# Optimization experiments

Measured on AMD Instinct MI355X. Metric: run time of the kernel, lower is better.

Reference implementation:

```python
import jax, jax.numpy as jnp
from jax import lax
import numpy as np


def hac_round(X, W):
    """Avg-linkage HAC build+cut rounding of fractional SDP matrix X (D,D).
    Returns the 0/1 symmetric round_matrix with 1-diagonal."""
    D = X.shape[0]
    dt = X.dtype
    MAXD = jnp.max(jnp.abs(X)) * 1000.0  # _MAX_DIST sentinel
    max_sim = jnp.max(X)                 # max_similarity passed by forward()
    tril_mask = jnp.tril(jnp.ones((D, D), dtype=bool))
    # use_similarities=True branch: Y = MAXD*tril + (max_sim - X).triu(1)
    Y = jnp.where(tril_mask, MAXD, max_sim - X)
    values = jnp.min(Y, axis=1)
    indices = jnp.argmin(Y, axis=1)
    parents = jnp.arange(2 * D - 1)
    p2i = jnp.arange(2 * D - 1)   # parent_to_idx
    i2p = jnp.arange(D)           # idx_to_parent
    cs = jnp.ones(2 * D - 1, dtype=dt)
    energy = jnp.zeros(2 * D - 1, dtype=dt)
    clustering = jnp.zeros((2 * D - 1, D), dtype=dt)
    clustering = clustering.at[jnp.arange(D), jnp.arange(D)].set(jnp.arange(1, D + 1, dtype=dt))
    R = jnp.eye(D, dtype=dt)

    def body(i, st):
        Y, values, indices, parents, p2i, i2p, cs, energy, clustering, R = st
        max_node = D + i
        m1 = jnp.argmin(values)
        m2 = indices[m1]
        p1 = i2p[p2i[i2p[m1]]]
        p2 = i2p[p2i[i2p[m2]]]
        parents = parents.at[p1].set(max_node).at[p2].set(max_node)
        i2p = i2p.at[m1].set(max_node)
        p2i = p2i.at[max_node].set(m1)
        max_mask = Y == MAXD
        cs1, cs2 = cs[p1], cs[p2]
        ncs = cs1 + cs2
        cs = cs.at[max_node].set(ncs)
        # weighted average-linkage merged distances
        newv = (jnp.minimum(Y[m1, :], Y[:, m1]) * cs1 + jnp.minimum(Y[:, m2], Y[m2, :]) * cs2) / ncs
        Y = Y.at[:, m1].set(newv).at[m1, :].set(newv)
        Y = jnp.where(max_mask, MAXD, Y)
        Y = Y.at[:, m2].set(MAXD).at[m2, :].set(MAXD)
        values = values.at[m2].set(MAXD)
        vmask = values == MAXD
        values = jnp.where(vmask, MAXD, jnp.min(Y, axis=1))
        indices = jnp.argmin(Y, axis=1)
        # cut decision for the new internal node
        crow = clustering[p1] + clustering[p2]
        leaf = crow > 0                      # membership of new cluster
        lf = leaf.astype(dt)
        merge_e = lf @ (W @ lf)              # sum of W over leaf x leaf pairs
        e_sum = energy[p1] + energy[p2]
        take = merge_e >= e_sum
        energy = energy.at[max_node].set(jnp.where(take, merge_e, e_sum))
        crow = jnp.where(take & leaf, (max_node).astype(dt), crow)
        clustering = clustering.at[max_node].set(crow)
        R = jnp.where(take & (leaf[:, None] & leaf[None, :]), jnp.asarray(1.0, dt), R)
        return (Y, values, indices, parents, p2i, i2p, cs, energy, clustering, R)

    st = (Y, values, indices, parents, p2i, i2p, cs, energy, clustering, R)
    st = lax.fori_loop(0, D - 1, body, st)
    return st[-1]


def setup_inputs() -> dict:
    key = jax.random.key(0)
    k1, k2 = jax.random.split(key)
    D = 1024
    A = jax.random.uniform(k1, (D, D), dtype=jnp.float32)
    X = 0.5 * (A + A.T)                      # symmetric fractional decisions
    X = X.at[jnp.arange(D), jnp.arange(D)].set(1.0)  # 1-diagonal
    W = jnp.triu(jax.random.normal(k2, (D, D), dtype=jnp.float32), 1)  # triu(1) weights
    return {"X": X, "W": W}


def reference(X, W):
    # straight-through estimator: hard rounded solution, identity gradient w.r.t. X
    R = hac_round(X, W)
    return X + lax.stop_gradient(R - X)
```

## Files before the change

kernel.cpp:

```cpp
#include <hip/hip_runtime.h>
#include <stdint.h>

#define D 1024

typedef unsigned long long u64;
typedef unsigned int u32;

__device__ __forceinline__ u32 enc_f(float f) {
    u32 b = __float_as_uint(f);
    return (b & 0x80000000u) ? ~b : (b | 0x80000000u);
}
__device__ __forceinline__ float dec_f(u32 u) {
    u32 b = (u & 0x80000000u) ? (u ^ 0x80000000u) : ~u;
    return __uint_as_float(b);
}

__global__ void k_maxred(const float* __restrict__ X, u32* scal) {
    float mx = -INFINITY, ma = 0.f;
    int stride = gridDim.x * blockDim.x;
    for (int i = blockIdx.x * blockDim.x + threadIdx.x; i < D * D; i += stride) {
        float v = X[i];
        mx = fmaxf(mx, v);
        ma = fmaxf(ma, fabsf(v));
    }
    for (int o = 32; o; o >>= 1) {
        mx = fmaxf(mx, __shfl_xor(mx, o));
        ma = fmaxf(ma, __shfl_xor(ma, o));
    }
    if ((threadIdx.x & 63) == 0) {
        atomicMax(&scal[0], enc_f(mx));
        atomicMax(&scal[1], enc_f(ma));
    }
}

__global__ void k_init(const float* __restrict__ X, const float* __restrict__ W,
                       float* __restrict__ dist, float* __restrict__ cross,
                       const u32* __restrict__ scal) {
    int idx = blockIdx.x * blockDim.x + threadIdx.x;
    if (idx >= D * D) return;
    float max_sim = dec_f(scal[0]);
    float MAXD = __fmul_rn(dec_f(scal[1]), 1000.0f);
    int i = idx >> 10, j = idx & (D - 1);
    float x = X[idx];
    dist[idx] = (i == j) ? MAXD : __fsub_rn(max_sim, x);
    cross[idx] = (i == j) ? 0.0f : (W[idx] + W[j * D + i]);
}

__global__ void k_rowmin(const float* __restrict__ dist, float* __restrict__ values_g,
                         int* __restrict__ indices_g, const u32* __restrict__ scal) {
    int r = blockIdx.x;
    int lane = threadIdx.x;
    float MAXD = __fmul_rn(dec_f(scal[1]), 1000.0f);
    u64 best = ((u64)__float_as_uint(MAXD) << 32);
    const float* row = dist + (size_t)r * D;
    for (int j = lane; j < D; j += 64) {
        if (j > r) {
            u64 k = ((u64)__float_as_uint(row[j]) << 32) | (u32)j;
            if (k < best) best = k;
        }
    }
    for (int o = 32; o; o >>= 1) {
        u64 k2 = __shfl_xor(best, o);
        if (k2 < best) best = k2;
    }
    if (lane == 0) {
        values_g[r] = __uint_as_float((u32)(best >> 32));
        indices_g[r] = (int)(best & 0xffffffffu);
    }
}

__global__ void __launch_bounds__(1024) k_hac(
        float* __restrict__ dist, float* __restrict__ cross,
        const float* __restrict__ values_g, const int* __restrict__ indices_g,
        int* __restrict__ labels_g, const u32* __restrict__ scal) {
    __shared__ __align__(16) float values_l[D];
    __shared__ float values_stage[D];
    __shared__ int indices_l[D];
    __shared__ __align__(16) float newv_l[D];
    __shared__ float cs_l[D];
    __shared__ unsigned char dead_l[D];
    __shared__ unsigned char marked_l[D];
    __shared__ int slot_l[D];
    __shared__ int label_l[D];
    __shared__ double within_l[D];
    __shared__ double energy_l[D];
    __shared__ int rlist[2][D];
    __shared__ int nrec[2];
    __shared__ u64 s_best[2];
    __shared__ float s_cross12;
    __shared__ int s_takeP, s_m1P, s_labP;

    const int t = threadIdx.x;
    const int lane = t & 63, wid = t >> 6;
    const float MAXD = __fmul_rn(dec_f(scal[1]), 1000.0f);
    const u32 MAXDb = __float_as_uint(MAXD);

    values_l[t] = values_g[t];
    indices_l[t] = indices_g[t];
    cs_l[t] = 1.0f;
    dead_l[t] = 0;
    marked_l[t] = 0;
    slot_l[t] = t;
    label_l[t] = t;
    within_l[t] = 0.0;
    energy_l[t] = 0.0;
    if (t == 0) {
        s_takeP = 0; s_m1P = -1; s_labP = 0;
        nrec[0] = 0; nrec[1] = 0;
        s_best[0] = ~0ull; s_best[1] = ~0ull;
    }
    __syncthreads();
    {
        u64 key = ((u64)__float_as_uint(values_l[t]) << 32) | ((u32)t << 10) |
                  (u32)indices_l[t];
        for (int o = 32; o; o >>= 1) {
            u64 k2 = __shfl_xor(key, o);
            if (k2 < key) key = k2;
        }
        if (lane == 0) atomicMin(&s_best[0], key);
    }
    __syncthreads();

    for (int it = 0; it < D - 1; ++it) {
        const int cb = it & 1, pb = cb ^ 1;

        const u64 bk = s_best[cb];
        const int m1 = (int)((bk >> 10) & 1023);
        const int m2 = (int)(bk & 1023);
        const float cs1 = cs_l[m1], cs2 = cs_l[m2];
        const float ncs = __fadd_rn(cs1, cs2);
        const int pm1 = s_m1P;
        if (t == 0) s_best[pb] = ~0ull;

        if (marked_l[t]) { values_l[t] = values_stage[t]; marked_l[t] = 0; }
        if (t == m2) {
            dead_l[m2] = 1;
            values_l[m2] = MAXD;
            indices_l[m2] = 0;
        }
        const bool alive = !dead_l[t];

        float d1, d2, c1, c2;
        if (alive || t == m2) {
            d1 = dist[(size_t)m1 * D + t];
            d2 = dist[(size_t)m2 * D + t];
            c1 = cross[(size_t)m1 * D + t];
            c2 = cross[(size_t)m2 * D + t];
        }

        {
            int sl = slot_l[t];
            if (s_takeP && sl == pm1) label_l[t] = s_labP;
            if (sl == m2) slot_l[t] = m1;
        }

        float nv = MAXD, ncx = 0.0f;
        bool do_st = false;
        {
            if (t == m2) s_cross12 = c1;
            if (alive && t != m1) {
                nv = __fdiv_rn(__fadd_rn(__fmul_rn(d1, cs1), __fmul_rn(d2, cs2)), ncs);
                ncx = c1 + c2;
                dist[(size_t)m1 * D + t] = nv;
                cross[(size_t)m1 * D + t] = ncx;
                do_st = true;
            }
            newv_l[t] = nv;
        }
        {
            float v = values_l[t];
            if (t == m1) {
                values_l[t] = MAXD;
                marked_l[t] = 1;
            } else if (alive && v < MAXD) {
                int idx = indices_l[t];
                if (idx == m2) {
                    rlist[cb][atomicAdd(&nrec[cb], 1)] = t;
                    values_l[t] = MAXD;
                    marked_l[t] = 1;
                } else if (idx == m1) {
                    if (nv <= v) values_l[t] = nv;
                    else {
                        rlist[cb][atomicAdd(&nrec[cb], 1)] = t;
                        values_l[t] = MAXD;
                        marked_l[t] = 1;
                    }
                } else if (t < m1) {
                    if (nv < v) { values_l[t] = nv; indices_l[t] = m1; }
                    else if (nv == v && m1 < idx) indices_l[t] = m1;
                }
            }
        }
        __syncthreads();

        if (do_st) {
            dist[(size_t)t * D + m1] = nv;
            cross[(size_t)t * D + m1] = ncx;
        }
        if (t == m1) cs_l[m1] = ncs;
        const int n = nrec[cb];
        if (t == 0) nrec[pb] = 0;

        if (wid == 0) {
            if (lane == 0) {
                double merge_e = within_l[m1] + within_l[m2] + (double)s_cross12;
                double e_sum = energy_l[m1] + energy_l[m2];
                int take = (merge_e >= e_sum) ? 1 : 0;
                within_l[m1] = merge_e;
                energy_l[m1] = take ? merge_e : e_sum;
                s_takeP = take;
                s_m1P = m1;
                s_labP = D + it;
            }
            const float4* v4 = (const float4*)values_l;
            u64 bb = ~0ull;
#pragma unroll
            for (int c = 0; c < 4; ++c) {
                int fi = lane + 64 * c;
                float4 q = v4[fi];
                int b = fi << 2;
                u64 k;
                k = ((u64)__float_as_uint(q.x) << 32) | (u32)(b + 0); if (k < bb) bb = k;
                k = ((u64)__float_as_uint(q.y) << 32) | (u32)(b + 1); if (k < bb) bb = k;
                k = ((u64)__float_as_uint(q.z) << 32) | (u32)(b + 2); if (k < bb) bb = k;
                k = ((u64)__float_as_uint(q.w) << 32) | (u32)(b + 3); if (k < bb) bb = k;
            }
            for (int o = 32; o; o >>= 1) {
                u64 k2 = __shfl_xor(bb, o);
                if (k2 < bb) bb = k2;
            }
            if (lane == 0) {
                int r = (int)(bb & 1023);
                int idx = indices_l[r];
                atomicMin(&s_best[pb],
                          (bb & 0xffffffff00000000ull) | ((u32)r << 10) | (u32)idx);
            }
        } else if (wid == 1) {
            u64 bb = ((u64)MAXDb << 32);
            const float4* nv4 = (const float4*)newv_l;
            for (int c = lane; c < D / 4; c += 64) {
                float4 q = nv4[c];
                int j0 = c << 2;
#pragma unroll
                for (int e = 0; e < 4; ++e) {
                    int j = j0 + e;
                    float dv = (e == 0) ? q.x : (e == 1) ? q.y : (e == 2) ? q.z : q.w;
                    if (j > m1) {
                        u64 k = ((u64)__float_as_uint(dv) << 32) | (u32)j;
                        if (k < bb) bb = k;
                    }
                }
            }
            for (int o = 32; o; o >>= 1) {
                u64 k2 = __shfl_xor(bb, o);
                if (k2 < bb) bb = k2;
            }
            if (lane == 0) {
                values_stage[m1] = __uint_as_float((u32)(bb >> 32));
                indices_l[m1] = (int)(bb & 0xffffffffu);
                atomicMin(&s_best[pb],
                          (bb & 0xffffffff00000000ull) | ((u32)m1 << 10) | (bb & 1023));
            }
        } else {
            for (int q = wid - 2; q < n; q += 14) {
                const int r = rlist[cb][q];
                const float subst = newv_l[r];
                u64 bb = ((u64)MAXDb << 32);
                const float4* row4 = (const float4*)(dist + (size_t)r * D);
                for (int c = lane; c < D / 4; c += 64) {
                    float4 q4 = row4[c];
                    int j0 = c << 2;
#pragma unroll
                    for (int e = 0; e < 4; ++e) {
                        int j = j0 + e;
                        float dv = (e == 0) ? q4.x : (e == 1) ? q4.y : (e == 2) ? q4.z : q4.w;
                        if (j == m1) dv = subst;
                        if (j > r && !dead_l[j]) {
                            u64 k = ((u64)__float_as_uint(dv) << 32) | (u32)j;
                            if (k < bb) bb = k;
                        }
                    }
                }
                for (int o = 32; o; o >>= 1) {
                    u64 k2 = __shfl_xor(bb, o);
                    if (k2 < bb) bb = k2;
                }
                if (lane == 0) {
                    values_stage[r] = __uint_as_float((u32)(bb >> 32));
                    indices_l[r] = (int)(bb & 0xffffffffu);
                    atomicMin(&s_best[pb],
                              (bb & 0xffffffff00000000ull) | ((u32)r << 10) | (bb & 1023));
                }
            }
        }
        __syncthreads();
    }

    {
        int lab = label_l[t];
        if (s_takeP && slot_l[t] == s_m1P) lab = s_labP;
        labels_g[t] = lab;
    }
}

__global__ void k_out(const int* __restrict__ labels, float* __restrict__ out) {
    int idx = blockIdx.x * blockDim.x + threadIdx.x;
    if (idx >= D * D) return;
    int i = idx >> 10, j = idx & (D - 1);
    out[idx] = (i == j || labels[i] == labels[j]) ? 1.0f : 0.0f;
}

extern "C" void kernel_launch(void* const* d_in, const int* in_sizes, int n_in,
                              void* d_out, int out_size, void* d_ws, size_t ws_size,
                              hipStream_t stream) {
    const float* X = (const float*)d_in[0];
    const float* W = (const float*)d_in[1];

    char* ws = (char*)d_ws;
    const size_t MAT_BYTES = (size_t)D * D * sizeof(float);
    float* dist = (float*)ws;
    float* cross = (float*)(ws + MAT_BYTES);
    float* values_g = (float*)(ws + 2 * MAT_BYTES);
    int* indices_g = (int*)(ws + 2 * MAT_BYTES + 4096);
    int* labels_g = (int*)(ws + 2 * MAT_BYTES + 8192);
    u32* scal = (u32*)(ws + 2 * MAT_BYTES + 12288);

    hipMemsetAsync(scal, 0, 2 * sizeof(u32), stream);
    k_maxred<<<256, 256, 0, stream>>>(X, scal);
    k_init<<<(D * D) / 256, 256, 0, stream>>>(X, W, dist, cross, scal);
    k_rowmin<<<D, 64, 0, stream>>>(dist, values_g, indices_g, scal);
    k_hac<<<1, 1024, 0, stream>>>(dist, cross, values_g, indices_g, labels_g, scal);
    k_out<<<(D * D) / 256, 256, 0, stream>>>(labels_g, (float*)d_out);
}
```

Before: 3.489 ms.

## Restructure HAC kernel to 256 threads owning four rows each

Shrinks the single-block HAC kernel from 1024 to 256 threads, with each thread owning four rows. Per-row values, indices and alive flags move into registers, and the global argmin is computed per thread and merged by shuffle plus atomicMin, so the separate wave-0 scan of shared values goes away. Dead columns are now handled by writing MAXD into column m2 of dist instead of checking a shared dead array, and the rescans that did not reach wave 1 now use a mailbox handoff. This cuts barrier cost and shared-memory traffic on the serial critical path, but leaves fewer waves to cover memory latency and to share the row rescans.

```diff
diff --git a/kernel.cpp b/kernel.cpp
--- a/kernel.cpp
+++ b/kernel.cpp
@@ -69,17 +69,14 @@
     }
 }
 
-__global__ void __launch_bounds__(1024) k_hac(
+__global__ void __launch_bounds__(256) k_hac(
         float* __restrict__ dist, float* __restrict__ cross,
         const float* __restrict__ values_g, const int* __restrict__ indices_g,
         int* __restrict__ labels_g, const u32* __restrict__ scal) {
-    __shared__ __align__(16) float values_l[D];
-    __shared__ float values_stage[D];
-    __shared__ int indices_l[D];
+    __shared__ float vmail[D];
+    __shared__ int imail[D];
     __shared__ __align__(16) float newv_l[D];
     __shared__ float cs_l[D];
-    __shared__ unsigned char dead_l[D];
-    __shared__ unsigned char marked_l[D];
     __shared__ int slot_l[D];
     __shared__ int label_l[D];
     __shared__ double within_l[D];
@@ -92,18 +89,26 @@
 
     const int t = threadIdx.x;
     const int lane = t & 63, wid = t >> 6;
+    const int r0 = 4 * t;
     const float MAXD = __fmul_rn(dec_f(scal[1]), 1000.0f);
     const u32 MAXDb = __float_as_uint(MAXD);
 
-    values_l[t] = values_g[t];
-    indices_l[t] = indices_g[t];
-    cs_l[t] = 1.0f;
-    dead_l[t] = 0;
-    marked_l[t] = 0;
-    slot_l[t] = t;
-    label_l[t] = t;
-    within_l[t] = 0.0;
-    energy_l[t] = 0.0;
+    float v[4];
+    int ix[4];
+    u32 aliveM = 0xFu;
+    bool resc[4] = {false, false, false, false};
+
+#pragma unroll
+    for (int e = 0; e < 4; ++e) {
+        int r = r0 + e;
+        v[e] = values_g[r];
+        ix[e] = indices_g[r];
+        cs_l[r] = 1.0f;
+        slot_l[r] = r;
+        label_l[r] = r;
+        within_l[r] = 0.0;
+        energy_l[r] = 0.0;
+    }
     if (t == 0) {
         s_takeP = 0; s_m1P = -1; s_labP = 0;
         nrec[0] = 0; nrec[1] = 0;
@@ -111,8 +116,12 @@
     }
     __syncthreads();
     {
-        u64 key = ((u64)__float_as_uint(values_l[t]) << 32) | ((u32)t << 10) |
-                  (u32)indices_l[t];
+        u64 key = ~0ull;
+#pragma unroll
+        for (int e = 0; e < 4; ++e) {
+            u64 k = ((u64)__float_as_uint(v[e]) << 32) | ((u32)(r0 + e) << 10) | (u32)ix[e];
+            if (k < key) key = k;
+        }
         for (int o = 32; o; o >>= 1) {
             u64 k2 = __shfl_xor(key, o);
             if (k2 < key) key = k2;
@@ -129,153 +138,169 @@
         const int m2 = (int)(bk & 1023);
         const float cs1 = cs_l[m1], cs2 = cs_l[m2];
         const float ncs = __fadd_rn(cs1, cs2);
-        const int pm1 = s_m1P;
-        if (t == 0) s_best[pb] = ~0ull;
-
-        if (marked_l[t]) { values_l[t] = values_stage[t]; marked_l[t] = 0; }
-        if (t == m2) {
-            dead_l[m2] = 1;
-            values_l[m2] = MAXD;
-            indices_l[m2] = 0;
-        }
-        const bool alive = !dead_l[t];
-
-        float d1, d2, c1, c2;
-        if (alive || t == m2) {
-            d1 = dist[(size_t)m1 * D + t];
-            d2 = dist[(size_t)m2 * D + t];
-            c1 = cross[(size_t)m1 * D + t];
-            c2 = cross[(size_t)m2 * D + t];
+        const int pm1 = s_m1P, ptake = s_takeP, plab = s_labP;
+
+#pragma unroll
+        for (int e = 0; e < 4; ++e) {
+            int r = r0 + e;
+            if (resc[e] || r == pm1) { v[e] = vmail[r]; ix[e] = imail[r]; resc[e] = false; }
+        }
+        const bool ownM2 = ((m2 >> 2) == t);
+        if (ownM2) {
+            int e2 = m2 & 3;
+            aliveM &= ~(1u << e2);
+            v[e2] = MAXD;
+            ix[e2] = 0;
+        }
+
+        const bool doLoad = (aliveM != 0u) || ownM2;
+        float4 d1, d2, c1, c2;
+        if (doLoad) {
+            d1 = *(const float4*)(dist + (size_t)m1 * D + r0);
+            d2 = *(const float4*)(dist + (size_t)m2 * D + r0);
+            c1 = *(const float4*)(cross + (size_t)m1 * D + r0);
+            c2 = *(const float4*)(cross + (size_t)m2 * D + r0);
+        }
+
+#pragma unroll
+        for (int e = 0; e < 4; ++e) {
+            int l = r0 + e;
+            int sl = slot_l[l];
+            if (ptake && sl == pm1) label_l[l] = plab;
+            if (sl == m2) slot_l[l] = m1;
+        }
+
+        float da[4] = {d1.x, d1.y, d1.z, d1.w};
+        float db[4] = {d2.x, d2.y, d2.z, d2.w};
+        float ea[4] = {c1.x, c1.y, c1.z, c1.w};
+        float eb[4] = {c2.x, c2.y, c2.z, c2.w};
+        if (ownM2) s_cross12 = ea[m2 & 3];
+
+        float nv[4], nc[4];
+#pragma unroll
+        for (int e = 0; e < 4; ++e) {
+            int j = r0 + e;
+            bool aj = (aliveM >> e) & 1u;
+            nv[e] = (aj && j != m1)
+                        ? __fdiv_rn(__fadd_rn(__fmul_rn(da[e], cs1), __fmul_rn(db[e], cs2)), ncs)
+                        : MAXD;
+            nc[e] = ea[e] + eb[e];
+        }
+        *(float4*)&newv_l[r0] = make_float4(nv[0], nv[1], nv[2], nv[3]);
+        if (aliveM) {
+            *(float4*)(dist + (size_t)m1 * D + r0) = make_float4(nv[0], nv[1], nv[2], nv[3]);
+            *(float4*)(cross + (size_t)m1 * D + r0) = make_float4(nc[0], nc[1], nc[2], nc[3]);
+        }
+
+        bool doR[4] = {false, false, false, false};
+#pragma unroll
+        for (int e = 0; e < 4; ++e) {
+            int r = r0 + e;
+            if (r == m1) continue;
+            if (((aliveM >> e) & 1u) && v[e] < MAXD) {
+                if (ix[e] == m2) {
+                    doR[e] = true;
+                } else if (ix[e] == m1) {
+                    if (nv[e] <= v[e]) v[e] = nv[e];
+                    else doR[e] = true;
+                } else if (r < m1) {
+                    if (nv[e] < v[e]) { v[e] = nv[e]; ix[e] = m1; }
+                    else if (nv[e] == v[e] && m1 < ix[e]) ix[e] = m1;
+                }
+            }
+            if (doR[e]) {
+                rlist[cb][atomicAdd(&nrec[cb], 1)] = r;
+                resc[e] = true;
+            }
         }
 
         {
-            int sl = slot_l[t];
-            if (s_takeP && sl == pm1) label_l[t] = s_labP;
-            if (sl == m2) slot_l[t] = m1;
-        }
-
-        float nv = MAXD, ncx = 0.0f;
-        bool do_st = false;
-        {
-            if (t == m2) s_cross12 = c1;
-            if (alive && t != m1) {
-                nv = __fdiv_rn(__fadd_rn(__fmul_rn(d1, cs1), __fmul_rn(d2, cs2)), ncs);
-                ncx = c1 + c2;
-                dist[(size_t)m1 * D + t] = nv;
-                cross[(size_t)m1 * D + t] = ncx;
-                do_st = true;
-            }
-            newv_l[t] = nv;
-        }
-        {
-            float v = values_l[t];
-            if (t == m1) {
-                values_l[t] = MAXD;
-                marked_l[t] = 1;
-            } else if (alive && v < MAXD) {
-                int idx = indices_l[t];
-                if (idx == m2) {
-                    rlist[cb][atomicAdd(&nrec[cb], 1)] = t;
-                    values_l[t] = MAXD;
-                    marked_l[t] = 1;
-                } else if (idx == m1) {
-                    if (nv <= v) values_l[t] = nv;
-                    else {
-                        rlist[cb][atomicAdd(&nrec[cb], 1)] = t;
-                        values_l[t] = MAXD;
-                        marked_l[t] = 1;
+            u64 key = ~0ull;
+#pragma unroll
+            for (int e = 0; e < 4; ++e) {
+                int r = r0 + e;
+                if (r == m1 || doR[e]) continue;
+                u64 k = ((u64)__float_as_uint(v[e]) << 32) | ((u32)r << 10) | (u32)ix[e];
+                if (k < key) key = k;
+            }
+            for (int o = 32; o; o >>= 1) {
+                u64 k2 = __shfl_xor(key, o);
+                if (k2 < key) key = k2;
+            }
+            if (lane == 0) atomicMin(&s_best[pb], key);
+        }
+        __syncthreads();
+
+        if (aliveM) {
+#pragma unroll
+            for (int e = 0; e < 4; ++e) {
+                int j = r0 + e;
+                if ((aliveM >> e) & 1u) {
+                    dist[(size_t)j * D + m1] = nv[e];
+                    cross[(size_t)j * D + m1] = nc[e];
+                    dist[(size_t)j * D + m2] = MAXD;
+                }
+            }
+        }
+        if (ownM2) dist[(size_t)m1 * D + m2] = MAXD;
+        if ((m1 >> 2) == t) cs_l[m1] = ncs;
+        if (t == 0) {
+            s_best[cb] = ~0ull;
+            nrec[pb] = 0;
+            double merge_e = within_l[m1] + within_l[m2] + (double)s_cross12;
+            double e_sum = energy_l[m1] + energy_l[m2];
+            int take = (merge_e >= e_sum) ? 1 : 0;
+            within_l[m1] = merge_e;
+            energy_l[m1] = take ? merge_e : e_sum;
+            s_takeP = take;
+            s_m1P = m1;
+            s_labP = D + it;
+        }
+        if (wid == 1) {
+            u64 bb = ((u64)MAXDb << 32);
+            const float4* nv4 = (const float4*)newv_l;
+#pragma unroll
+            for (int c = 0; c < 4; ++c) {
+                float4 q = nv4[lane + 64 * c];
+                int j0 = 4 * (lane + 64 * c);
+                float qa[4] = {q.x, q.y, q.z, q.w};
+#pragma unroll
+                for (int e = 0; e < 4; ++e) {
+                    int j = j0 + e;
+                    if (j > m1) {
+                        u64 k = ((u64)__float_as_uint(qa[e]) << 32) | (u32)j;
+                        if (k < bb) bb = k;
                     }
-                } else if (t < m1) {
-                    if (nv < v) { values_l[t] = nv; indices_l[t] = m1; }
-                    else if (nv == v && m1 < idx) indices_l[t] = m1;
-                }
-            }
-        }
-        __syncthreads();
-
-        if (do_st) {
-            dist[(size_t)t * D + m1] = nv;
-            cross[(size_t)t * D + m1] = ncx;
-        }
-        if (t == m1) cs_l[m1] = ncs;
-        const int n = nrec[cb];
-        if (t == 0) nrec[pb] = 0;
-
-        if (wid == 0) {
-            if (lane == 0) {
-                double merge_e = within_l[m1] + within_l[m2] + (double)s_cross12;
-                double e_sum = energy_l[m1] + energy_l[m2];
-                int take = (merge_e >= e_sum) ? 1 : 0;
-                within_l[m1] = merge_e;
-                energy_l[m1] = take ? merge_e : e_sum;
-                s_takeP = take;
-                s_m1P = m1;
-                s_labP = D + it;
-            }
-            const float4* v4 = (const float4*)values_l;
-            u64 bb = ~0ull;
-#pragma unroll
-            for (int c = 0; c < 4; ++c) {
-                int fi = lane + 64 * c;
-                float4 q = v4[fi];
-                int b = fi << 2;
-                u64 k;
-                k = ((u64)__float_as_uint(q.x) << 32) | (u32)(b + 0); if (k < bb) bb = k;
-                k = ((u64)__float_as_uint(q.y) << 32) | (u32)(b + 1); if (k < bb) bb = k;
-                k = ((u64)__float_as_uint(q.z) << 32) | (u32)(b + 2); if (k < bb) bb = k;
-                k = ((u64)__float_as_uint(q.w) << 32) | (u32)(b + 3); if (k < bb) bb = k;
+                }
             }
             for (int o = 32; o; o >>= 1) {
                 u64 k2 = __shfl_xor(bb, o);
                 if (k2 < bb) bb = k2;
             }
             if (lane == 0) {
-                int r = (int)(bb & 1023);
-                int idx = indices_l[r];
-                atomicMin(&s_best[pb],
-                          (bb & 0xffffffff00000000ull) | ((u32)r << 10) | (u32)idx);
-            }
-        } else if (wid == 1) {
-            u64 bb = ((u64)MAXDb << 32);
-            const float4* nv4 = (const float4*)newv_l;
-            for (int c = lane; c < D / 4; c += 64) {
-                float4 q = nv4[c];
-                int j0 = c << 2;
-#pragma unroll
-                for (int e = 0; e < 4; ++e) {
-                    int j = j0 + e;
-                    float dv = (e == 0) ? q.x : (e == 1) ? q.y : (e == 2) ? q.z : q.w;
-                    if (j > m1) {
-                        u64 k = ((u64)__float_as_uint(dv) << 32) | (u32)j;
-                        if (k < bb) bb = k;
-                    }
-                }
-            }
-            for (int o = 32; o; o >>= 1) {
-                u64 k2 = __shfl_xor(bb, o);
-                if (k2 < bb) bb = k2;
-            }
-            if (lane == 0) {
-                values_stage[m1] = __uint_as_float((u32)(bb >> 32));
-                indices_l[m1] = (int)(bb & 0xffffffffu);
+                vmail[m1] = __uint_as_float((u32)(bb >> 32));
+                imail[m1] = (int)(bb & 0xffffffffu);
                 atomicMin(&s_best[pb],
                           (bb & 0xffffffff00000000ull) | ((u32)m1 << 10) | (bb & 1023));
             }
-        } else {
-            for (int q = wid - 2; q < n; q += 14) {
+        }
+        {
+            const int n = nrec[cb];
+            for (int q = wid; q < n; q += 4) {
                 const int r = rlist[cb][q];
                 const float subst = newv_l[r];
                 u64 bb = ((u64)MAXDb << 32);
                 const float4* row4 = (const float4*)(dist + (size_t)r * D);
-                for (int c = lane; c < D / 4; c += 64) {
-                    float4 q4 = row4[c];
-                    int j0 = c << 2;
+#pragma unroll
+                for (int c = 0; c < 4; ++c) {
+                    float4 q4 = row4[lane + 64 * c];
+                    int j0 = 4 * (lane + 64 * c);
+                    float qa[4] = {q4.x, q4.y, q4.z, q4.w};
 #pragma unroll
                     for (int e = 0; e < 4; ++e) {
                         int j = j0 + e;
-                        float dv = (e == 0) ? q4.x : (e == 1) ? q4.y : (e == 2) ? q4.z : q4.w;
-                        if (j == m1) dv = subst;
-                        if (j > r && !dead_l[j]) {
+                        float dv = (j == m1) ? subst : qa[e];
+                        if (j > r && j != m2) {
                             u64 k = ((u64)__float_as_uint(dv) << 32) | (u32)j;
                             if (k < bb) bb = k;
                         }
@@ -286,8 +311,8 @@
                     if (k2 < bb) bb = k2;
                 }
                 if (lane == 0) {
-                    values_stage[r] = __uint_as_float((u32)(bb >> 32));
-                    indices_l[r] = (int)(bb & 0xffffffffu);
+                    vmail[r] = __uint_as_float((u32)(bb >> 32));
+                    imail[r] = (int)(bb & 0xffffffffu);
                     atomicMin(&s_best[pb],
                               (bb & 0xffffffff00000000ull) | ((u32)r << 10) | (bb & 1023));
                 }
@@ -296,10 +321,12 @@
         __syncthreads();
     }
 
-    {
-        int lab = label_l[t];
-        if (s_takeP && slot_l[t] == s_m1P) lab = s_labP;
-        labels_g[t] = lab;
+#pragma unroll
+    for (int e = 0; e < 4; ++e) {
+        int l = r0 + e;
+        int lab = label_l[l];
+        if (s_takeP && slot_l[l] == s_m1P) lab = s_labP;
+        labels_g[l] = lab;
     }
 }
 
@@ -329,6 +356,6 @@
     k_maxred<<<256, 256, 0, stream>>>(X, scal);
     k_init<<<(D * D) / 256, 256, 0, stream>>>(X, W, dist, cross, scal);
     k_rowmin<<<D, 64, 0, stream>>>(dist, values_g, indices_g, scal);
-    k_hac<<<1, 1024, 0, stream>>>(dist, cross, values_g, indices_g, labels_g, scal);
+    k_hac<<<1, 256, 0, stream>>>(dist, cross, values_g, indices_g, labels_g, scal);
     k_out<<<(D * D) / 256, 256, 0, stream>>>(labels_g, (float*)d_out);
 }
```

After: 5.386 ms. 54.4% more time.
